# Performance work log

Measured on AMD Instinct MI355X. Metric: run time of the kernel, lower is better.

## Reference

```python
import jax, jax.numpy as jnp
import numpy as np

N = 100000   # support / query points
H = 32       # neighbors per query
C = 64       # channels
K = 15       # kernel points (sum(shell_sizes)=1+14)
RADIUS = 1.0
SIGMA = 0.3
INF = 1.0e6  # shadow-point coordinate


def setup_inputs() -> dict:
    key = jax.random.key(0)
    k0, k1, k2, k3, k4, k5 = jax.random.split(key, 6)
    s_pts = jax.random.uniform(k0, (N, 3), dtype=jnp.float32) * (2.0 * RADIUS)
    q_pts = jax.random.uniform(k1, (N, 3), dtype=jnp.float32) * (2.0 * RADIUS)
    s_feats = jax.random.normal(k2, (N, C), dtype=jnp.float32)
    neighb_inds = jax.random.randint(k3, (N, H), 0, N)
    # kaiming_uniform_(a=sqrt(5)) on (K, C): bound = 1/sqrt(fan_in) = 1/sqrt(C)
    bound = 1.0 / np.sqrt(C)
    weights = jax.random.uniform(k4, (K, C), dtype=jnp.float32, minval=-bound, maxval=bound)
    # kernel point dispositions within the ball of RADIUS; center point fixed at origin
    kernel_points = jax.random.normal(k5, (K, 3), dtype=jnp.float32) * (0.5 * RADIUS)
    kernel_points = kernel_points.at[0].set(0.0)
    return {
        "q_pts": q_pts,
        "s_pts": s_pts,
        "s_feats": s_feats,
        "neighb_inds": neighb_inds,
        "weights": weights,
        "kernel_points": kernel_points,
    }


def reference(q_pts, s_pts, s_feats, neighb_inds, weights, kernel_points):
    M = q_pts.shape[0]
    Cc = s_feats.shape[1]
    # pad with shadow point (far away) / zero feature row so out-of-range idx == N
    s_pts_pad = jnp.concatenate([s_pts, jnp.full((1, 3), INF, s_pts.dtype)], axis=0)
    s_feats_pad = jnp.concatenate([s_feats, jnp.zeros((1, Cc), s_feats.dtype)], axis=0)

    neighbor_feats = s_feats_pad[neighb_inds]                 # [M, H, C]
    neighbors = s_pts_pad[neighb_inds] - q_pts[:, None, :]    # [M, H, 3]

    # squared distance to each kernel point, nearest-kernel assignment
    diffs = neighbors[:, :, None, :] - kernel_points[None, None, :, :]  # [M, H, K, 3]
    sq_dists = jnp.sum(diffs * diffs, axis=-1)                # [M, H, K]
    nn_sq_dists = jnp.min(sq_dists, axis=2)                   # [M, H]
    neighbors_1nn = jnp.argmin(sq_dists, axis=2)              # [M, H]

    # linear influence
    influence = jnp.clip(1.0 - jnp.sqrt(nn_sq_dists) / SIGMA, 0.0)  # [M, H]

    # depthwise (Cmid=0): gather per-kernel-point weights, modulate, sum over neighbors
    neighbors_weights = weights[neighbors_1nn] * influence[..., None]  # [M, H, C]
    output_feats = jnp.sum(neighbor_feats * neighbors_weights, axis=1)  # [M, C]
    return output_feats
```

## Files before the change

kernel.cpp:

```cpp
#include <hip/hip_runtime.h>

#define H 32
#define C 64
#define K 15
#define SIGMA 0.3f
#define WAVES 4
#define QPW 4

__global__ __launch_bounds__(256) void kpconv_kernel(
    const float* __restrict__ q_pts,
    const float* __restrict__ s_pts,
    const float* __restrict__ s_feats,
    const int*   __restrict__ inds,
    const float* __restrict__ weights,
    const float* __restrict__ kpts,
    float*       __restrict__ out,
    int N)
{
    __shared__ float2 list[WAVES][QPW][34];

    const int tid  = threadIdx.x;
    const int wave = tid >> 6;
    const int lane = tid & 63;
    const int half = lane >> 5;
    const int hl   = lane & 31;

    float kp[K * 3];
    #pragma unroll
    for (int i = 0; i < K * 3; ++i) kp[i] = kpts[i];

    const int qBase = (blockIdx.x * WAVES + wave) * QPW;

    int c0 = 0, c1 = 0, c2 = 0, c3 = 0;

    #pragma unroll
    for (int p = 0; p < 2; ++p) {
        const int m = qBase + p * 2 + half;
        float infl = 0.0f;
        int   packed = 0;
        if (m < N) {
            const int idx = inds[m * H + hl];
            if (idx >= 0 && idx < N) {
                const float qx = q_pts[m * 3 + 0];
                const float qy = q_pts[m * 3 + 1];
                const float qz = q_pts[m * 3 + 2];
                const float nx = s_pts[idx * 3 + 0] - qx;
                const float ny = s_pts[idx * 3 + 1] - qy;
                const float nz = s_pts[idx * 3 + 2] - qz;
                float best = 1e30f;
                int   kbest = 0;
                #pragma unroll
                for (int k = 0; k < K; ++k) {
                    const float dx = nx - kp[k * 3 + 0];
                    const float dy = ny - kp[k * 3 + 1];
                    const float dz = nz - kp[k * 3 + 2];
                    const float d2 = dx * dx + dy * dy + dz * dz;
                    if (d2 < best) { best = d2; kbest = k; }
                }
                infl = 1.0f - __builtin_amdgcn_sqrtf(best) * (1.0f / SIGMA);
                if (infl < 0.0f) infl = 0.0f;
                packed = idx | (kbest << 20);
            }
        }
        const unsigned long long ball = __ballot(infl > 0.0f);
        const unsigned int lo = (unsigned int)(ball & 0xFFFFFFFFu);
        const unsigned int hi = (unsigned int)(ball >> 32);
        const unsigned int maskH = half ? hi : lo;
        const int rank = __popc(maskH & ((1u << hl) - 1u));
        if (infl > 0.0f)
            list[wave][p * 2 + half][rank] = make_float2(__int_as_float(packed), infl);
        if (p == 0) { c0 = __popc(lo); c1 = __popc(hi); }
        else        { c2 = __popc(lo); c3 = __popc(hi); }
    }

    const int q  = lane >> 4;
    const int ql = lane & 15;
    const int cq = (q < 2) ? (q == 0 ? c0 : c1) : (q == 2 ? c2 : c3);
    int maxc = c0 > c1 ? c0 : c1;
    if (c2 > maxc) maxc = c2;
    if (c3 > maxc) maxc = c3;

    float4 acc = make_float4(0.0f, 0.0f, 0.0f, 0.0f);
    for (int i = 0; i < maxc; i += 2) {
        if (i < cq) {
            const float4 pf = *(const float4*)&list[wave][q][i];
            const int   p0   = __float_as_int(pf.x);
            const float f0   = pf.y;
            const bool  has1 = (i + 1) < cq;
            const int   p1   = has1 ? __float_as_int(pf.z) : 0;
            const float f1   = has1 ? pf.w : 0.0f;
            const float4 a0 = *(const float4*)(s_feats + (size_t)(p0 & 0xFFFFF) * C + ql * 4);
            const float4 w0 = *(const float4*)(weights + (p0 >> 20) * C + ql * 4);
            const float4 a1 = *(const float4*)(s_feats + (size_t)(p1 & 0xFFFFF) * C + ql * 4);
            const float4 w1 = *(const float4*)(weights + (p1 >> 20) * C + ql * 4);
            acc.x += a0.x * w0.x * f0;  acc.y += a0.y * w0.y * f0;
            acc.z += a0.z * w0.z * f0;  acc.w += a0.w * w0.w * f0;
            acc.x += a1.x * w1.x * f1;  acc.y += a1.y * w1.y * f1;
            acc.z += a1.z * w1.z * f1;  acc.w += a1.w * w1.w * f1;
        }
    }

    const int mq = qBase + q;
    if (mq < N)
        *(float4*)(out + (size_t)mq * C + ql * 4) = acc;
}

extern "C" void kernel_launch(void* const* d_in, const int* in_sizes, int n_in,
                              void* d_out, int out_size, void* d_ws, size_t ws_size,
                              hipStream_t stream) {
    const float* q_pts   = (const float*)d_in[0];
    const float* s_pts   = (const float*)d_in[1];
    const float* s_feats = (const float*)d_in[2];
    const int*   inds    = (const int*)d_in[3];
    const float* weights = (const float*)d_in[4];
    const float* kpts    = (const float*)d_in[5];
    float* out = (float*)d_out;

    const int N = in_sizes[0] / 3;
    const int qpb = WAVES * QPW;
    const int blocks = (N + qpb - 1) / qpb;
    kpconv_kernel<<<blocks, 256, 0, stream>>>(q_pts, s_pts, s_feats, inds,
                                              weights, kpts, out, N);
}
```

Baseline: 33.36 us.

## Split KPConv into neighbor-compaction and feature-gather kernels via workspace

Splits the fused kernel into two launches. The first computes nearest kernel points and influences, then writes compacted per-query entry lists and counts to a global workspace. The second reads those lists and does the feature/weight gather-accumulate with a per-query loop bound instead of a wave-wide max. This aims to remove divergence and the wave-wide max-count loop and lets each phase run at its own occupancy, at the cost of an extra launch and a global round trip of up to N*32*8 bytes. The fused kernel is kept as a fallback when the workspace is too small.

```diff
diff --git a/kernel.cpp b/kernel.cpp
--- a/kernel.cpp
+++ b/kernel.cpp
@@ -4,10 +4,111 @@
 #define C 64
 #define K 15
 #define SIGMA 0.3f
+
+__global__ __launch_bounds__(256) void kpconv_phaseA(
+    const float* __restrict__ q_pts,
+    const float* __restrict__ s_pts,
+    const int*   __restrict__ inds,
+    const float* __restrict__ kpts,
+    int*         __restrict__ cnt,
+    float2*      __restrict__ entries,
+    int N)
+{
+    const int tid  = threadIdx.x;
+    const int wave = tid >> 6;
+    const int lane = tid & 63;
+    const int half = lane >> 5;
+    const int hl   = lane & 31;
+
+    float kp[K * 3];
+    #pragma unroll
+    for (int i = 0; i < K * 3; ++i) kp[i] = kpts[i];
+
+    const int m = (blockIdx.x * 4 + wave) * 2 + half;
+
+    float infl   = 0.0f;
+    int   packed = 0;
+    if (m < N) {
+        const int idx = inds[m * H + hl];
+        if (idx >= 0 && idx < N) {
+            const float qx = q_pts[m * 3 + 0];
+            const float qy = q_pts[m * 3 + 1];
+            const float qz = q_pts[m * 3 + 2];
+            const float nx = s_pts[idx * 3 + 0] - qx;
+            const float ny = s_pts[idx * 3 + 1] - qy;
+            const float nz = s_pts[idx * 3 + 2] - qz;
+            float best = 1e30f;
+            int   kbest = 0;
+            #pragma unroll
+            for (int k = 0; k < K; ++k) {
+                const float dx = nx - kp[k * 3 + 0];
+                const float dy = ny - kp[k * 3 + 1];
+                const float dz = nz - kp[k * 3 + 2];
+                const float d2 = dx * dx + dy * dy + dz * dz;
+                if (d2 < best) { best = d2; kbest = k; }
+            }
+            infl = 1.0f - __builtin_amdgcn_sqrtf(best) * (1.0f / SIGMA);
+            if (infl < 0.0f) infl = 0.0f;
+            packed = idx | (kbest << 20);
+        }
+    }
+
+    const unsigned long long ball = __ballot(infl > 0.0f);
+    const unsigned int lo = (unsigned int)(ball & 0xFFFFFFFFu);
+    const unsigned int hi = (unsigned int)(ball >> 32);
+    const unsigned int maskH = half ? hi : lo;
+    const int rank = __popc(maskH & ((1u << hl) - 1u));
+
+    if (infl > 0.0f)
+        entries[(size_t)m * 32 + rank] = make_float2(__int_as_float(packed), infl);
+    if (hl == 0 && m < N)
+        cnt[m] = __popc(maskH);
+}
+
+__global__ __launch_bounds__(256) void kpconv_phaseB(
+    const float*  __restrict__ s_feats,
+    const float*  __restrict__ weights,
+    const int*    __restrict__ cnt,
+    const float2* __restrict__ entries,
+    float*        __restrict__ out,
+    int N)
+{
+    const int tid  = threadIdx.x;
+    const int wave = tid >> 6;
+    const int lane = tid & 63;
+    const int q    = lane >> 4;
+    const int ql   = lane & 15;
+
+    const int mq = (blockIdx.x * 4 + wave) * 4 + q;
+    const int cq = (mq < N) ? cnt[mq] : 0;
+
+    const float4* row = (const float4*)(entries + (size_t)mq * 32);
+    float4 acc = make_float4(0.0f, 0.0f, 0.0f, 0.0f);
+
+    for (int i = 0; i < cq; i += 2) {
+        const float4 pf = row[i >> 1];
+        const int   p0   = __float_as_int(pf.x);
+        const float f0   = pf.y;
+        const bool  has1 = (i + 1) < cq;
+        const int   p1   = has1 ? __float_as_int(pf.z) : 0;
+        const float f1   = has1 ? pf.w : 0.0f;
+        const float4 a0 = *(const float4*)(s_feats + (size_t)(p0 & 0xFFFFF) * C + ql * 4);
+        const float4 w0 = *(const float4*)(weights + (p0 >> 20) * C + ql * 4);
+        const float4 a1 = *(const float4*)(s_feats + (size_t)(p1 & 0xFFFFF) * C + ql * 4);
+        const float4 w1 = *(const float4*)(weights + (p1 >> 20) * C + ql * 4);
+        acc.x += a0.x * w0.x * f0;  acc.y += a0.y * w0.y * f0;
+        acc.z += a0.z * w0.z * f0;  acc.w += a0.w * w0.w * f0;
+        acc.x += a1.x * w1.x * f1;  acc.y += a1.y * w1.y * f1;
+        acc.z += a1.z * w1.z * f1;  acc.w += a1.w * w1.w * f1;
+    }
+
+    if (mq < N)
+        *(float4*)(out + (size_t)mq * C + ql * 4) = acc;
+}
+
 #define WAVES 4
 #define QPW 4
-
-__global__ __launch_bounds__(256) void kpconv_kernel(
+__global__ __launch_bounds__(256) void kpconv_fused(
     const float* __restrict__ q_pts,
     const float* __restrict__ s_pts,
     const float* __restrict__ s_feats,
@@ -30,7 +131,6 @@
     for (int i = 0; i < K * 3; ++i) kp[i] = kpts[i];
 
     const int qBase = (blockIdx.x * WAVES + wave) * QPW;
-
     int c0 = 0, c1 = 0, c2 = 0, c3 = 0;
 
     #pragma unroll
@@ -117,8 +217,23 @@
     float* out = (float*)d_out;
 
     const int N = in_sizes[0] / 3;
-    const int qpb = WAVES * QPW;
-    const int blocks = (N + qpb - 1) / qpb;
-    kpconv_kernel<<<blocks, 256, 0, stream>>>(q_pts, s_pts, s_feats, inds,
-                                              weights, kpts, out, N);
-}
+
+    const size_t entOff  = 1 << 20;
+    const size_t wsNeed  = entOff + (size_t)N * 32 * sizeof(float2);
+
+    if (ws_size >= wsNeed) {
+        int*    cnt     = (int*)d_ws;
+        float2* entries = (float2*)((char*)d_ws + entOff);
+        const int blocksA = (N + 7) / 8;
+        const int blocksB = (N + 15) / 16;
+        kpconv_phaseA<<<blocksA, 256, 0, stream>>>(q_pts, s_pts, inds, kpts,
+                                                   cnt, entries, N);
+        kpconv_phaseB<<<blocksB, 256, 0, stream>>>(s_feats, weights, cnt,
+                                                   entries, out, N);
+    } else {
+        const int qpb = WAVES * QPW;
+        const int blocks = (N + qpb - 1) / qpb;
+        kpconv_fused<<<blocks, 256, 0, stream>>>(q_pts, s_pts, s_feats, inds,
+                                                 weights, kpts, out, N);
+    }
+}
```

After: 42.33 us. +26.9%, slower.
